# Performance work log

Hardware: AMD Instinct MI355X
Metric: run time of the kernel (lower is better)

## Reference

```python
import jax, jax.numpy as jnp
import numpy as np


def _conv1x1(x, W, b):
    # x: (B,C,H,W), W: (O,C), b: (O,)
    return jnp.einsum('bchw,oc->bohw', x, W) + b[None, :, None, None]


def _maxpool2(x):
    B, C, H, W = x.shape
    return x.reshape(B, C, H // 2, 2, W // 2, 2).max(axis=(3, 5))


def setup_inputs() -> dict:
    key = jax.random.key(0)
    ks = jax.random.split(key, 6)
    B, C, H, W = 8, 1024, 64, 64
    DI, DO = 512, 1024
    std = 0.01  # matches nn.init.normal_(std=0.01)
    return {
        'x': jax.random.normal(ks[0], (B, C, H, W), dtype=jnp.float32),
        'W_theta': std * jax.random.normal(ks[1], (DI, C), dtype=jnp.float32),
        'b_theta': jnp.zeros((DI,), jnp.float32),
        'W_phi': std * jax.random.normal(ks[2], (DI, C), dtype=jnp.float32),
        'b_phi': jnp.zeros((DI,), jnp.float32),
        'W_g': std * jax.random.normal(ks[3], (DI, C), dtype=jnp.float32),
        'b_g': jnp.zeros((DI,), jnp.float32),
        'W_out': std * jax.random.normal(ks[4], (DO, DI), dtype=jnp.float32),
        'b_out': jnp.zeros((DO,), jnp.float32),
    }


def reference(x, W_theta, b_theta, W_phi, b_phi, W_g, b_g, W_out, b_out):
    B, C, H, W = x.shape
    di = W_theta.shape[0]
    scale = di ** (-0.5)
    # queries from full-res map: (B, di, N) with N = H*W
    theta = _conv1x1(x, W_theta, b_theta).reshape(B, di, H * W)
    # keys/values from 2x2-maxpooled map: (B, di, M), M = (H/2)*(W/2)
    px = _maxpool2(x)
    phi = _conv1x1(px, W_phi, b_phi).reshape(B, di, -1)
    g = _conv1x1(px, W_g, b_g).reshape(B, di, -1)
    # attention: (B, N, M)
    logits = jnp.einsum('bdn,bdm->bnm', theta, phi) * scale
    p = jax.nn.softmax(logits, axis=-1)
    # aggregate values: (B, di, N) -> (B, di, H, W)
    t = jnp.einsum('bdm,bnm->bdn', g, p).reshape(B, di, H, W)
    y = _conv1x1(t, W_out, b_out)
    return y + x
```

## Files before the change

### kernel.cpp

```cpp
#include <hip/hip_runtime.h>
#include <hip/hip_bf16.h>
#include <stdint.h>

typedef __bf16 bf16;
typedef __bf16 bf16x8 __attribute__((ext_vector_type(8)));
typedef __bf16 bf16x4 __attribute__((ext_vector_type(4)));
typedef float f32x4 __attribute__((ext_vector_type(4)));

#define GLOAD_LDS16(gptr, lptr)                                                        \
  __builtin_amdgcn_global_load_lds((const __attribute__((address_space(1))) void*)(gptr), \
                                   (__attribute__((address_space(3))) void*)(lptr), 16, 0, 0)

__global__ __launch_bounds__(256) void cast_f2b(const float* __restrict__ in,
                                                bf16* __restrict__ out, int n) {
  int i = (blockIdx.x * 256 + threadIdx.x) * 4;
  if (i >= n) return;
  const float4 v = *(const float4*)(in + i);
  bf16x4 o;
  o[0] = (bf16)v.x; o[1] = (bf16)v.y; o[2] = (bf16)v.z; o[3] = (bf16)v.w;
  *(bf16x4*)(out + i) = o;
}

__global__ __launch_bounds__(256) void prep_kernel(const float* __restrict__ x,
                                                   bf16* __restrict__ xbT,
                                                   bf16* __restrict__ pxT) {
  const int b = blockIdx.y;
  x   += (size_t)b * 1024 * 4096;
  xbT += (size_t)b * 4096 * 1024;
  pxT += (size_t)b * 1024 * 1024;
  const int bid = blockIdx.x;
  const int h0 = bid & 31, ct = bid >> 5;
  const int tid = threadIdx.x;
  __shared__ float tile[32][129];
  const float* xs = x + (size_t)(ct * 32) * 4096 + h0 * 128;
#pragma unroll
  for (int e = 0; e < 16; ++e) {
    int idx = e * 256 + tid;
    int c = idx >> 7, n = idx & 127;
    tile[c][n] = xs[(size_t)c * 4096 + n];
  }
  __syncthreads();
  bf16* xo = xbT + (size_t)(h0 * 128) * 1024 + ct * 32;
#pragma unroll
  for (int e = 0; e < 16; ++e) {
    int idx = e * 256 + tid;
    int n = idx >> 5, c = idx & 31;
    xo[(size_t)n * 1024 + c] = (bf16)tile[c][n];
  }
  bf16* po = pxT + (size_t)(h0 * 32) * 1024 + ct * 32;
#pragma unroll
  for (int e = 0; e < 4; ++e) {
    int idx = e * 256 + tid;
    int m = idx >> 5, c = idx & 31;
    float v = fmaxf(fmaxf(tile[c][2 * m], tile[c][2 * m + 1]),
                    fmaxf(tile[c][64 + 2 * m], tile[c][64 + 2 * m + 1]));
    po[(size_t)m * 1024 + c] = (bf16)v;
  }
}

__global__ __launch_bounds__(256) void rowsum_k(const bf16* __restrict__ P,
                                                float* __restrict__ rs) {
  const int row = blockIdx.x * 4 + (threadIdx.x >> 6);
  const int lane = threadIdx.x & 63;
  const bf16* Pr = P + (size_t)row * 1024;
  bf16x8 v0 = *(const bf16x8*)(Pr + lane * 16);
  bf16x8 v1 = *(const bf16x8*)(Pr + lane * 16 + 8);
  float s = 0.f;
#pragma unroll
  for (int e = 0; e < 8; ++e) s += (float)v0[e] + (float)v1[e];
#pragma unroll
  for (int o = 32; o > 0; o >>= 1) s += __shfl_xor(s, o);
  if (lane == 0) rs[row] = s;
}

template <int EPI>
__global__ __launch_bounds__(512, 1) void gemm256(
    const bf16* __restrict__ A, long long sA, int lda,
    const bf16* __restrict__ B, long long sB, int ldb,
    void* __restrict__ Cv, long long sC, int ldc, int K,
    const float* __restrict__ bias,
    const float* __restrict__ resid, long long sResid, float scale) {
  const int z = blockIdx.z;
  A += (size_t)z * sA;
  B += (size_t)z * sB;
  const int tid = threadIdx.x;
  const int w = tid >> 6, lane = tid & 63;
  const int r16 = lane & 15, q4 = lane >> 4;
  const int wm = w >> 2, wn = w & 3;
  const long long tileM = (long long)blockIdx.x * 256;
  const long long tileN = (long long)blockIdx.y * 256;

  __shared__ bf16 As[4][8192];
  __shared__ bf16 Bs[4][8192];

  f32x4 acc[8][4] = {};

  const int srow = tid >> 2;
  const int skb  = (tid & 3) ^ ((srow >> 1) & 3);
  const char* Ag = (const char*)A + ((size_t)(tileM + srow) * lda + skb * 8) * 2;
  const char* Bg = (const char*)B + ((size_t)(tileN + srow) * ldb + skb * 8) * 2;
  const size_t a128 = (size_t)128 * lda * 2;
  const size_t b128 = (size_t)128 * ldb * 2;

  auto stA = [&](int T) {
    bf16* d = &As[T & 3][w * 512];
    const char* s = Ag + (size_t)T * 64;
    GLOAD_LDS16(s, d);
    GLOAD_LDS16(s + a128, d + 4096);
  };
  auto stB = [&](int T) {
    bf16* d = &Bs[T & 3][w * 512];
    const char* s = Bg + (size_t)T * 64;
    GLOAD_LDS16(s, d);
    GLOAD_LDS16(s + b128, d + 4096);
  };

  stA(0); stB(0); stA(1); stB(1);
  const int NT = K >> 5;

  for (int T = 0; T < NT; ++T) {
    if (T + 2 < NT) stA(T + 2);
    if (T + 2 < NT)      asm volatile("s_waitcnt vmcnt(6)" ::: "memory");
    else if (T + 1 < NT) asm volatile("s_waitcnt vmcnt(4)" ::: "memory");
    else                 asm volatile("s_waitcnt vmcnt(0)" ::: "memory");
    __builtin_amdgcn_s_barrier();
    asm volatile("" ::: "memory");

    const char* Asl = (const char*)&As[T & 3][0];
    const char* Bsl = (const char*)&Bs[T & 3][0];
    bf16x8 bf_[4];
#pragma unroll
    for (int ni = 0; ni < 4; ++ni) {
      const int row = wn * 64 + ni * 16 + r16;
      bf_[ni] = *(const bf16x8*)(Bsl + row * 64 + ((q4 ^ ((row >> 1) & 3)) << 4));
    }
    bf16x8 af[4];
#pragma unroll
    for (int mi = 0; mi < 4; ++mi) {
      const int row = wm * 128 + mi * 16 + r16;
      af[mi] = *(const bf16x8*)(Asl + row * 64 + ((q4 ^ ((row >> 1) & 3)) << 4));
    }
    __builtin_amdgcn_s_setprio(1);
#pragma unroll
    for (int mi = 0; mi < 4; ++mi)
#pragma unroll
      for (int ni = 0; ni < 4; ++ni)
        acc[mi][ni] = __builtin_amdgcn_mfma_f32_16x16x32_bf16(af[mi], bf_[ni], acc[mi][ni], 0, 0, 0);
    __builtin_amdgcn_s_setprio(0);

    if (T + 2 < NT) stB(T + 2);
#pragma unroll
    for (int mi = 0; mi < 4; ++mi) {
      const int row = wm * 128 + 64 + mi * 16 + r16;
      af[mi] = *(const bf16x8*)(Asl + row * 64 + ((q4 ^ ((row >> 1) & 3)) << 4));
    }
    __builtin_amdgcn_s_setprio(1);
#pragma unroll
    for (int mi = 0; mi < 4; ++mi)
#pragma unroll
      for (int ni = 0; ni < 4; ++ni)
        acc[4 + mi][ni] = __builtin_amdgcn_mfma_f32_16x16x32_bf16(af[mi], bf_[ni], acc[4 + mi][ni], 0, 0, 0);
    __builtin_amdgcn_s_setprio(0);
  }

  if constexpr (EPI == 4) {
    float* C = (float*)Cv + (size_t)z * sC;
    const float* rz = resid + (size_t)z * sResid;
#pragma unroll
    for (int a = 0; a < 8; ++a) {
      const int row0 = (int)tileM + wm * 128 + a * 16 + q4 * 4;
#pragma unroll
      for (int ni = 0; ni < 4; ++ni) {
        const int col = (int)tileN + wn * 64 + ni * 16 + r16;
#pragma unroll
        for (int r = 0; r < 4; ++r)
          C[(size_t)(row0 + r) * ldc + col] =
              acc[a][ni][r] + bias[row0 + r] + rz[(size_t)(row0 + r) * ldc + col];
      }
    }
  } else if constexpr (EPI == 5) {
    bf16* C = (bf16*)Cv + (size_t)z * sC;
#pragma unroll
    for (int a = 0; a < 8; ++a) {
      const int row0 = (int)tileM + wm * 128 + a * 16 + q4 * 4;
#pragma unroll
      for (int ni = 0; ni < 4; ++ni) {
        const int col = (int)tileN + wn * 64 + ni * 16 + r16;
#pragma unroll
        for (int r = 0; r < 4; ++r)
          C[(size_t)(row0 + r) * ldc + col] = (bf16)__expf(acc[a][ni][r]);
      }
    }
  } else if constexpr (EPI == 7) {
    bf16* C = (bf16*)Cv + (size_t)z * sC;
    const float* rsp = bias + (size_t)z * 4096;
#pragma unroll
    for (int a = 0; a < 8; ++a) {
      const int row0 = (int)tileM + wm * 128 + a * 16 + q4 * 4;
      float inv[4];
#pragma unroll
      for (int r = 0; r < 4; ++r) inv[r] = 1.0f / rsp[row0 + r];
#pragma unroll
      for (int ni = 0; ni < 4; ++ni) {
        const int col = (int)tileN + wn * 64 + ni * 16 + r16;
#pragma unroll
        for (int r = 0; r < 4; ++r)
          C[(size_t)(row0 + r) * ldc + col] = (bf16)(acc[a][ni][r] * inv[r]);
      }
    }
  } else {
    bf16* C = (bf16*)Cv + (size_t)z * sC;
#pragma unroll
    for (int a = 0; a < 8; ++a) {
      const int row0 = (int)tileM + wm * 128 + a * 16 + q4 * 4;
#pragma unroll
      for (int ni = 0; ni < 4; ++ni) {
        const int col = (int)tileN + wn * 64 + ni * 16 + r16;
        const float badd = bias[col];
#pragma unroll
        for (int r = 0; r < 4; ++r)
          C[(size_t)(row0 + r) * ldc + col] = (bf16)((acc[a][ni][r] + badd) * scale);
      }
    }
  }
}

template <int EPI>
__global__ __launch_bounds__(256) void gemm_bt(
    const bf16* __restrict__ A, long long sA, int lda,
    const bf16* __restrict__ B, long long sB, int ldb,
    void* __restrict__ Cv, long long sC, int ldc, int K,
    const float* __restrict__ bias,
    const float* __restrict__ resid, long long sResid, float scale) {
  const int z = blockIdx.z;
  A += (size_t)z * sA;
  B += (size_t)z * sB;
  const int tid = threadIdx.x;
  const int w = tid >> 6, lane = tid & 63;
  const int r16 = lane & 15, q4 = lane >> 4;
  const long long tileM = (long long)blockIdx.x * 128;
  const long long tileN = (long long)blockIdx.y * 128;

  __shared__ bf16 As[2][128 * 32];
  __shared__ bf16 Bs[2][128 * 32];

  f32x4 acc[4][4] = {};

  const int srow = tid >> 2;
  const int soff = (tid & 3) * 16;
  const char* Ag0 = (const char*)A + ((size_t)(tileM + srow) * lda) * 2 + soff;
  const char* Bg0 = (const char*)B + ((size_t)(tileN + srow) * ldb) * 2 + soff;
  const size_t arow64 = (size_t)64 * lda * 2;
  const size_t brow64 = (size_t)64 * ldb * 2;

  auto stage = [&](int buf, int k0) {
    const char* a = Ag0 + (size_t)k0 * 2;
    const char* b = Bg0 + (size_t)k0 * 2;
    bf16* al = &As[buf][w * 512];
    bf16* bl = &Bs[buf][w * 512];
    GLOAD_LDS16(a, al);
    GLOAD_LDS16(a + arow64, al + 2048);
    GLOAD_LDS16(b, bl);
    GLOAD_LDS16(b + brow64, bl + 2048);
  };

  const int wr = (w >> 1) * 64, wc = (w & 1) * 64;
  const int nt = K >> 5;
  stage(0, 0);
  __syncthreads();
  int cur = 0;
  for (int t = 0; t < nt; ++t) {
    if (t + 1 < nt) stage(cur ^ 1, (t + 1) * 32);
    bf16x8 af[4], bfv[4];
#pragma unroll
    for (int f = 0; f < 4; ++f) {
      af[f]  = *(const bf16x8*)&As[cur][(wr + f * 16 + r16) * 32 + q4 * 8];
      bfv[f] = *(const bf16x8*)&Bs[cur][(wc + f * 16 + r16) * 32 + q4 * 8];
    }
#pragma unroll
    for (int i = 0; i < 4; ++i)
#pragma unroll
      for (int j = 0; j < 4; ++j)
        acc[i][j] = __builtin_amdgcn_mfma_f32_16x16x32_bf16(af[i], bfv[j], acc[i][j], 0, 0, 0);
    __syncthreads();
    cur ^= 1;
  }

  bf16* C = (bf16*)Cv + (size_t)z * sC;
#pragma unroll
  for (int i = 0; i < 4; ++i) {
    const int row0 = (int)tileM + wr + i * 16 + q4 * 4;
#pragma unroll
    for (int j = 0; j < 4; ++j) {
      const int col = (int)tileN + wc + j * 16 + r16;
      float badd = 0.f;
      if constexpr (EPI == 1) badd = bias[col];
#pragma unroll
      for (int r = 0; r < 4; ++r) {
        float v = acc[i][j][r];
        if constexpr (EPI == 1) v = (v + badd) * scale;
        if constexpr (EPI == 2) v += bias[row0 + r];
        C[(size_t)(row0 + r) * ldc + col] = (bf16)v;
      }
    }
  }
}

extern "C" void kernel_launch(void* const* d_in, const int* in_sizes, int n_in,
                              void* d_out, int out_size, void* d_ws, size_t ws_size,
                              hipStream_t stream) {
  const float* x  = (const float*)d_in[0];
  const float* Wt = (const float*)d_in[1];
  const float* bt = (const float*)d_in[2];
  const float* Wp = (const float*)d_in[3];
  const float* bp = (const float*)d_in[4];
  const float* Wg = (const float*)d_in[5];
  const float* bg = (const float*)d_in[6];
  const float* Wo = (const float*)d_in[7];
  const float* bo = (const float*)d_in[8];
  float* out = (float*)d_out;

  const size_t MB = 1024ull * 1024ull;
  char* ws = (char*)d_ws;
  bf16* WtB = (bf16*)(ws + 0 * MB);
  bf16* WpB = (bf16*)(ws + 1 * MB);
  bf16* WgB = (bf16*)(ws + 2 * MB);
  bf16* WoB = (bf16*)(ws + 3 * MB);

  cast_f2b<<<512, 256, 0, stream>>>(Wt, WtB, 512 * 1024);
  cast_f2b<<<512, 256, 0, stream>>>(Wp, WpB, 512 * 1024);
  cast_f2b<<<512, 256, 0, stream>>>(Wg, WgB, 512 * 1024);
  cast_f2b<<<512, 256, 0, stream>>>(Wo, WoB, 1024 * 512);

  const float SCALE = 0.044194173824159216f;

  auto run_g6 = [&](int nb, int b0, bf16* tT) {
    gemm256<4><<<dim3(4, 16, nb), 512, 0, stream>>>(WoB, 0, 512, tT, 4096ll * 512, 512,
                                                    out + (size_t)b0 * 1024 * 4096,
                                                    1024ll * 4096, 4096, 512,
                                                    bo, x + (size_t)b0 * 1024 * 4096,
                                                    1024ll * 4096, 1.f);
  };

  if (ws_size >= 164 * MB) {
    bf16* pxT    = (bf16*)(ws + 4 * MB);
    bf16* phiT   = (bf16*)(ws + 20 * MB);
    bf16* g      = (bf16*)(ws + 28 * MB);
    bf16* thetaT = (bf16*)(ws + 36 * MB);
    bf16* tT     = (bf16*)(ws + 68 * MB);
    bf16* xbT    = (bf16*)(ws + 100 * MB);
    bf16*  Pt   = (bf16*)d_out;
    float* rsum = (float*)((char*)d_out + 80 * MB);

    prep_kernel<<<dim3(1024, 8), 256, 0, stream>>>(x, xbT, pxT);
    gemm256<1><<<dim3(16, 2, 8), 512, 0, stream>>>(xbT, 4096ll * 1024, 1024, WtB, 0, 1024,
                                                   thetaT, 4096ll * 512, 512, 1024,
                                                   bt, nullptr, 0, SCALE);
    gemm_bt<1><<<dim3(8, 4, 8), 256, 0, stream>>>(pxT, 1024ll * 1024, 1024, WpB, 0, 1024,
                                                  phiT, 1024ll * 512, 512, 1024,
                                                  bp, nullptr, 0, 1.f);
    gemm_bt<2><<<dim3(4, 8, 8), 256, 0, stream>>>(WgB, 0, 1024, pxT, 1024ll * 1024, 1024,
                                                  g, 512ll * 1024, 1024, 1024,
                                                  bg, nullptr, 0, 1.f);
    gemm256<5><<<dim3(16, 4, 8), 512, 0, stream>>>(thetaT, 4096ll * 512, 512,
                                                   phiT, 1024ll * 512, 512,
                                                   Pt, 4096ll * 1024, 1024, 512,
                                                   nullptr, nullptr, 0, 1.f);
    rowsum_k<<<8192, 256, 0, stream>>>(Pt, rsum);
    gemm256<7><<<dim3(16, 2, 8), 512, 0, stream>>>(Pt, 4096ll * 1024, 1024,
                                                   g, 512ll * 1024, 1024,
                                                   tT, 4096ll * 512, 512, 1024,
                                                   rsum, nullptr, 0, 1.f);
    run_g6(8, 0, tT);
  } else if (ws_size >= 108 * MB) {
    bf16* pxT    = (bf16*)(ws + 4 * MB);
    bf16* phiT   = (bf16*)(ws + 20 * MB);
    bf16* g      = (bf16*)(ws + 28 * MB);
    bf16* thetaT = (bf16*)(ws + 36 * MB);
    bf16* tT     = (bf16*)(ws + 68 * MB);
    bf16* xbT    = (bf16*)(ws + 100 * MB);
    float* rsum = (float*)((char*)d_out + 80 * MB);
    for (int b = 0; b < 8; ++b) {
      prep_kernel<<<dim3(1024, 1), 256, 0, stream>>>(x + (size_t)b * 1024 * 4096, xbT,
                                                     pxT + (size_t)b * 1024 * 1024);
      gemm256<1><<<dim3(16, 2, 1), 512, 0, stream>>>(xbT, 0, 1024, WtB, 0, 1024,
                                                     thetaT + (size_t)b * 4096 * 512, 0, 512,
                                                     1024, bt, nullptr, 0, SCALE);
    }
    gemm_bt<1><<<dim3(8, 4, 8), 256, 0, stream>>>(pxT, 1024ll * 1024, 1024, WpB, 0, 1024,
                                                  phiT, 1024ll * 512, 512, 1024,
                                                  bp, nullptr, 0, 1.f);
    gemm_bt<2><<<dim3(4, 8, 8), 256, 0, stream>>>(WgB, 0, 1024, pxT, 1024ll * 1024, 1024,
                                                  g, 512ll * 1024, 1024, 1024,
                                                  bg, nullptr, 0, 1.f);
    for (int b = 0; b < 8; ++b) {
      bf16* Ptb = (bf16*)d_out + (size_t)b * 4096 * 1024;
      gemm256<5><<<dim3(16, 4, 1), 512, 0, stream>>>(thetaT + (size_t)b * 4096 * 512, 0, 512,
                                                     phiT + (size_t)b * 1024 * 512, 0, 512,
                                                     Ptb, 0, 1024, 512,
                                                     nullptr, nullptr, 0, 1.f);
      rowsum_k<<<1024, 256, 0, stream>>>(Ptb, rsum + (size_t)b * 4096);
      gemm256<7><<<dim3(16, 2, 1), 512, 0, stream>>>(Ptb, 0, 1024,
                                                     g + (size_t)b * 512 * 1024, 0, 1024,
                                                     tT + (size_t)b * 4096 * 512, 0, 512, 1024,
                                                     rsum + (size_t)b * 4096, nullptr, 0, 1.f);
    }
    run_g6(8, 0, tT);
  } else {
    float* rsum  = (float*)(ws + 4 * MB);
    bf16* pxT    = (bf16*)(ws + 5 * MB);
    bf16* phiT   = (bf16*)(ws + 7 * MB);
    bf16* g      = (bf16*)(ws + 8 * MB);
    bf16* thetaT = (bf16*)(ws + 9 * MB);
    bf16* tT     = (bf16*)(ws + 13 * MB);
    bf16* Pt     = (bf16*)(ws + 17 * MB);
    bf16* xbT    = (bf16*)(ws + 25 * MB);
    for (int b = 0; b < 8; ++b) {
      prep_kernel<<<dim3(1024, 1), 256, 0, stream>>>(x + (size_t)b * 1024 * 4096, xbT, pxT);
      gemm256<1><<<dim3(16, 2, 1), 512, 0, stream>>>(xbT, 0, 1024, WtB, 0, 1024,
                                                     thetaT, 0, 512, 1024,
                                                     bt, nullptr, 0, SCALE);
      gemm_bt<1><<<dim3(8, 4, 1), 256, 0, stream>>>(pxT, 0, 1024, WpB, 0, 1024,
                                                    phiT, 0, 512, 1024,
                                                    bp, nullptr, 0, 1.f);
      gemm_bt<2><<<dim3(4, 8, 1), 256, 0, stream>>>(WgB, 0, 1024, pxT, 0, 1024,
                                                    g, 0, 1024, 1024,
                                                    bg, nullptr, 0, 1.f);
      gemm256<5><<<dim3(16, 4, 1), 512, 0, stream>>>(thetaT, 0, 512, phiT, 0, 512,
                                                     Pt, 0, 1024, 512,
                                                     nullptr, nullptr, 0, 1.f);
      rowsum_k<<<1024, 256, 0, stream>>>(Pt, rsum);
      gemm256<7><<<dim3(16, 2, 1), 512, 0, stream>>>(Pt, 0, 1024, g, 0, 1024,
                                                     tT, 0, 512, 1024,
                                                     rsum, nullptr, 0, 1.f);
      run_g6(1, b, tT);
    }
  }
}
```

Baseline: 322.9 us.

## Shrink gemm256 tile to 128x256, double-buffer, fuse softmax row sums via atomics

The main GEMM kernel moves from 256x256 tiles with a 4-stage LDS ring to 128x256 tiles with a 2-stage buffer, which cuts LDS use and accumulator registers and raises the launch-bounds occupancy hint. Grids are doubled in M to match. The separate rowsum pass over the exp(P) matrix is removed, and row sums are now built in the exp epilogue with shuffle reductions and atomicAdd into a buffer zeroed by a new small kernel. The trade-off is less B-tile reuse per block, a full vmcnt(0) wait each iteration with less prefetch depth, and atomic contention on the row sums.

```diff
diff --git a/kernel.cpp b/kernel.cpp
--- a/kernel.cpp
+++ b/kernel.cpp
@@ -19,6 +19,11 @@
   bf16x4 o;
   o[0] = (bf16)v.x; o[1] = (bf16)v.y; o[2] = (bf16)v.z; o[3] = (bf16)v.w;
   *(bf16x4*)(out + i) = o;
+}
+
+__global__ __launch_bounds__(256) void zero_k(float* __restrict__ p, int n) {
+  int i = blockIdx.x * 256 + threadIdx.x;
+  if (i < n) p[i] = 0.f;
 }
 
 __global__ __launch_bounds__(256) void prep_kernel(const float* __restrict__ x,
@@ -58,28 +63,14 @@
   }
 }
 
-__global__ __launch_bounds__(256) void rowsum_k(const bf16* __restrict__ P,
-                                                float* __restrict__ rs) {
-  const int row = blockIdx.x * 4 + (threadIdx.x >> 6);
-  const int lane = threadIdx.x & 63;
-  const bf16* Pr = P + (size_t)row * 1024;
-  bf16x8 v0 = *(const bf16x8*)(Pr + lane * 16);
-  bf16x8 v1 = *(const bf16x8*)(Pr + lane * 16 + 8);
-  float s = 0.f;
-#pragma unroll
-  for (int e = 0; e < 8; ++e) s += (float)v0[e] + (float)v1[e];
-#pragma unroll
-  for (int o = 32; o > 0; o >>= 1) s += __shfl_xor(s, o);
-  if (lane == 0) rs[row] = s;
-}
-
 template <int EPI>
-__global__ __launch_bounds__(512, 1) void gemm256(
+__global__ __launch_bounds__(512, 4) void gemm256(
     const bf16* __restrict__ A, long long sA, int lda,
     const bf16* __restrict__ B, long long sB, int ldb,
     void* __restrict__ Cv, long long sC, int ldc, int K,
     const float* __restrict__ bias,
-    const float* __restrict__ resid, long long sResid, float scale) {
+    const float* __restrict__ resid, long long sResid, float scale,
+    float* __restrict__ rs_out) {
   const int z = blockIdx.z;
   A += (size_t)z * sA;
   B += (size_t)z * sB;
@@ -87,59 +78,48 @@
   const int w = tid >> 6, lane = tid & 63;
   const int r16 = lane & 15, q4 = lane >> 4;
   const int wm = w >> 2, wn = w & 3;
-  const long long tileM = (long long)blockIdx.x * 256;
+  const long long tileM = (long long)blockIdx.x * 128;
   const long long tileN = (long long)blockIdx.y * 256;
 
-  __shared__ bf16 As[4][8192];
-  __shared__ bf16 Bs[4][8192];
-
-  f32x4 acc[8][4] = {};
+  __shared__ bf16 As[2][4096];
+  __shared__ bf16 Bs[2][8192];
+
+  f32x4 acc[4][4] = {};
 
   const int srow = tid >> 2;
   const int skb  = (tid & 3) ^ ((srow >> 1) & 3);
   const char* Ag = (const char*)A + ((size_t)(tileM + srow) * lda + skb * 8) * 2;
   const char* Bg = (const char*)B + ((size_t)(tileN + srow) * ldb + skb * 8) * 2;
-  const size_t a128 = (size_t)128 * lda * 2;
   const size_t b128 = (size_t)128 * ldb * 2;
 
-  auto stA = [&](int T) {
-    bf16* d = &As[T & 3][w * 512];
-    const char* s = Ag + (size_t)T * 64;
-    GLOAD_LDS16(s, d);
-    GLOAD_LDS16(s + a128, d + 4096);
+  auto stage = [&](int T) {
+    const int sl = T & 1;
+    GLOAD_LDS16(Ag + (size_t)T * 64, &As[sl][w * 512]);
+    GLOAD_LDS16(Bg + (size_t)T * 64, &Bs[sl][w * 512]);
+    GLOAD_LDS16(Bg + (size_t)T * 64 + b128, &Bs[sl][4096 + w * 512]);
   };
-  auto stB = [&](int T) {
-    bf16* d = &Bs[T & 3][w * 512];
-    const char* s = Bg + (size_t)T * 64;
-    GLOAD_LDS16(s, d);
-    GLOAD_LDS16(s + b128, d + 4096);
-  };
-
-  stA(0); stB(0); stA(1); stB(1);
+
+  stage(0);
   const int NT = K >> 5;
 
   for (int T = 0; T < NT; ++T) {
-    if (T + 2 < NT) stA(T + 2);
-    if (T + 2 < NT)      asm volatile("s_waitcnt vmcnt(6)" ::: "memory");
-    else if (T + 1 < NT) asm volatile("s_waitcnt vmcnt(4)" ::: "memory");
-    else                 asm volatile("s_waitcnt vmcnt(0)" ::: "memory");
+    asm volatile("s_waitcnt vmcnt(0)" ::: "memory");
     __builtin_amdgcn_s_barrier();
     asm volatile("" ::: "memory");
-
-    const char* Asl = (const char*)&As[T & 3][0];
-    const char* Bsl = (const char*)&Bs[T & 3][0];
-    bf16x8 bf_[4];
+    if (T + 1 < NT) stage(T + 1);
+    const char* Asl = (const char*)&As[T & 1][0];
+    const char* Bsl = (const char*)&Bs[T & 1][0];
+    bf16x8 af[4], bf_[4];
+#pragma unroll
+    for (int mi = 0; mi < 4; ++mi) {
+      const int row = wm * 64 + mi * 16 + r16;
+      af[mi] = *(const bf16x8*)(Asl + row * 64 + ((q4 ^ ((row >> 1) & 3)) << 4));
+    }
 #pragma unroll
     for (int ni = 0; ni < 4; ++ni) {
       const int row = wn * 64 + ni * 16 + r16;
       bf_[ni] = *(const bf16x8*)(Bsl + row * 64 + ((q4 ^ ((row >> 1) & 3)) << 4));
     }
-    bf16x8 af[4];
-#pragma unroll
-    for (int mi = 0; mi < 4; ++mi) {
-      const int row = wm * 128 + mi * 16 + r16;
-      af[mi] = *(const bf16x8*)(Asl + row * 64 + ((q4 ^ ((row >> 1) & 3)) << 4));
-    }
     __builtin_amdgcn_s_setprio(1);
 #pragma unroll
     for (int mi = 0; mi < 4; ++mi)
@@ -147,28 +127,14 @@
       for (int ni = 0; ni < 4; ++ni)
         acc[mi][ni] = __builtin_amdgcn_mfma_f32_16x16x32_bf16(af[mi], bf_[ni], acc[mi][ni], 0, 0, 0);
     __builtin_amdgcn_s_setprio(0);
-
-    if (T + 2 < NT) stB(T + 2);
-#pragma unroll
-    for (int mi = 0; mi < 4; ++mi) {
-      const int row = wm * 128 + 64 + mi * 16 + r16;
-      af[mi] = *(const bf16x8*)(Asl + row * 64 + ((q4 ^ ((row >> 1) & 3)) << 4));
-    }
-    __builtin_amdgcn_s_setprio(1);
-#pragma unroll
-    for (int mi = 0; mi < 4; ++mi)
-#pragma unroll
-      for (int ni = 0; ni < 4; ++ni)
-        acc[4 + mi][ni] = __builtin_amdgcn_mfma_f32_16x16x32_bf16(af[mi], bf_[ni], acc[4 + mi][ni], 0, 0, 0);
-    __builtin_amdgcn_s_setprio(0);
   }
 
   if constexpr (EPI == 4) {
     float* C = (float*)Cv + (size_t)z * sC;
     const float* rz = resid + (size_t)z * sResid;
 #pragma unroll
-    for (int a = 0; a < 8; ++a) {
-      const int row0 = (int)tileM + wm * 128 + a * 16 + q4 * 4;
+    for (int a = 0; a < 4; ++a) {
+      const int row0 = (int)tileM + wm * 64 + a * 16 + q4 * 4;
 #pragma unroll
       for (int ni = 0; ni < 4; ++ni) {
         const int col = (int)tileN + wn * 64 + ni * 16 + r16;
@@ -180,23 +146,37 @@
     }
   } else if constexpr (EPI == 5) {
     bf16* C = (bf16*)Cv + (size_t)z * sC;
-#pragma unroll
-    for (int a = 0; a < 8; ++a) {
-      const int row0 = (int)tileM + wm * 128 + a * 16 + q4 * 4;
+    float* rsp = rs_out + (size_t)z * 4096;
+#pragma unroll
+    for (int a = 0; a < 4; ++a) {
+      const int row0 = (int)tileM + wm * 64 + a * 16 + q4 * 4;
+      float psum[4] = {0.f, 0.f, 0.f, 0.f};
 #pragma unroll
       for (int ni = 0; ni < 4; ++ni) {
         const int col = (int)tileN + wn * 64 + ni * 16 + r16;
 #pragma unroll
-        for (int r = 0; r < 4; ++r)
-          C[(size_t)(row0 + r) * ldc + col] = (bf16)__expf(acc[a][ni][r]);
+        for (int r = 0; r < 4; ++r) {
+          float e = __expf(acc[a][ni][r]);
+          psum[r] += e;
+          C[(size_t)(row0 + r) * ldc + col] = (bf16)e;
+        }
+      }
+#pragma unroll
+      for (int r = 0; r < 4; ++r) {
+        float v = psum[r];
+        v += __shfl_xor(v, 1);
+        v += __shfl_xor(v, 2);
+        v += __shfl_xor(v, 4);
+        v += __shfl_xor(v, 8);
+        if (r16 == 0) atomicAdd(&rsp[row0 + r], v);
       }
     }
   } else if constexpr (EPI == 7) {
     bf16* C = (bf16*)Cv + (size_t)z * sC;
     const float* rsp = bias + (size_t)z * 4096;
 #pragma unroll
-    for (int a = 0; a < 8; ++a) {
-      const int row0 = (int)tileM + wm * 128 + a * 16 + q4 * 4;
+    for (int a = 0; a < 4; ++a) {
+      const int row0 = (int)tileM + wm * 64 + a * 16 + q4 * 4;
       float inv[4];
 #pragma unroll
       for (int r = 0; r < 4; ++r) inv[r] = 1.0f / rsp[row0 + r];
@@ -211,8 +191,8 @@
   } else {
     bf16* C = (bf16*)Cv + (size_t)z * sC;
 #pragma unroll
-    for (int a = 0; a < 8; ++a) {
-      const int row0 = (int)tileM + wm * 128 + a * 16 + q4 * 4;
+    for (int a = 0; a < 4; ++a) {
+      const int row0 = (int)tileM + wm * 64 + a * 16 + q4 * 4;
 #pragma unroll
       for (int ni = 0; ni < 4; ++ni) {
         const int col = (int)tileN + wn * 64 + ni * 16 + r16;
@@ -230,8 +210,7 @@
     const bf16* __restrict__ A, long long sA, int lda,
     const bf16* __restrict__ B, long long sB, int ldb,
     void* __restrict__ Cv, long long sC, int ldc, int K,
-    const float* __restrict__ bias,
-    const float* __restrict__ resid, long long sResid, float scale) {
+    const float* __restrict__ bias, float scale) {
   const int z = blockIdx.z;
   A += (size_t)z * sA;
   B += (size_t)z * sB;
@@ -335,11 +314,11 @@
   const float SCALE = 0.044194173824159216f;
 
   auto run_g6 = [&](int nb, int b0, bf16* tT) {
-    gemm256<4><<<dim3(4, 16, nb), 512, 0, stream>>>(WoB, 0, 512, tT, 4096ll * 512, 512,
+    gemm256<4><<<dim3(8, 16, nb), 512, 0, stream>>>(WoB, 0, 512, tT, 4096ll * 512, 512,
                                                     out + (size_t)b0 * 1024 * 4096,
                                                     1024ll * 4096, 4096, 512,
                                                     bo, x + (size_t)b0 * 1024 * 4096,
-                                                    1024ll * 4096, 1.f);
+                                                    1024ll * 4096, 1.f, nullptr);
   };
 
   if (ws_size >= 164 * MB) {
@@ -353,24 +332,22 @@
     float* rsum = (float*)((char*)d_out + 80 * MB);
 
     prep_kernel<<<dim3(1024, 8), 256, 0, stream>>>(x, xbT, pxT);
-    gemm256<1><<<dim3(16, 2, 8), 512, 0, stream>>>(xbT, 4096ll * 1024, 1024, WtB, 0, 1024,
+    gemm256<1><<<dim3(32, 2, 8), 512, 0, stream>>>(xbT, 4096ll * 1024, 1024, WtB, 0, 1024,
                                                    thetaT, 4096ll * 512, 512, 1024,
-                                                   bt, nullptr, 0, SCALE);
+                                                   bt, nullptr, 0, SCALE, nullptr);
     gemm_bt<1><<<dim3(8, 4, 8), 256, 0, stream>>>(pxT, 1024ll * 1024, 1024, WpB, 0, 1024,
-                                                  phiT, 1024ll * 512, 512, 1024,
-                                                  bp, nullptr, 0, 1.f);
+                                                  phiT, 1024ll * 512, 512, 1024, bp, 1.f);
     gemm_bt<2><<<dim3(4, 8, 8), 256, 0, stream>>>(WgB, 0, 1024, pxT, 1024ll * 1024, 1024,
-                                                  g, 512ll * 1024, 1024, 1024,
-                                                  bg, nullptr, 0, 1.f);
-    gemm256<5><<<dim3(16, 4, 8), 512, 0, stream>>>(thetaT, 4096ll * 512, 512,
+                                                  g, 512ll * 1024, 1024, 1024, bg, 1.f);
+    zero_k<<<128, 256, 0, stream>>>(rsum, 32768);
+    gemm256<5><<<dim3(32, 4, 8), 512, 0, stream>>>(thetaT, 4096ll * 512, 512,
                                                    phiT, 1024ll * 512, 512,
                                                    Pt, 4096ll * 1024, 1024, 512,
-                                                   nullptr, nullptr, 0, 1.f);
-    rowsum_k<<<8192, 256, 0, stream>>>(Pt, rsum);
-    gemm256<7><<<dim3(16, 2, 8), 512, 0, stream>>>(Pt, 4096ll * 1024, 1024,
+                                                   nullptr, nullptr, 0, 1.f, rsum);
+    gemm256<7><<<dim3(32, 2, 8), 512, 0, stream>>>(Pt, 4096ll * 1024, 1024,
                                                    g, 512ll * 1024, 1024,
                                                    tT, 4096ll * 512, 512, 1024,
-                                                   rsum, nullptr, 0, 1.f);
+                                                   rsum, nullptr, 0, 1.f, nullptr);
     run_g6(8, 0, tT);
   } else if (ws_size >= 108 * MB) {
     bf16* pxT    = (bf16*)(ws + 4 * MB);
@@ -383,27 +360,27 @@
     for (int b = 0; b < 8; ++b) {
       prep_kernel<<<dim3(1024, 1), 256, 0, stream>>>(x + (size_t)b * 1024 * 4096, xbT,
                                                      pxT + (size_t)b * 1024 * 1024);
-      gemm256<1><<<dim3(16, 2, 1), 512, 0, stream>>>(xbT, 0, 1024, WtB, 0, 1024,
+      gemm256<1><<<dim3(32, 2, 1), 512, 0, stream>>>(xbT, 0, 1024, WtB, 0, 1024,
                                                      thetaT + (size_t)b * 4096 * 512, 0, 512,
-                                                     1024, bt, nullptr, 0, SCALE);
+                                                     1024, bt, nullptr, 0, SCALE, nullptr);
     }
     gemm_bt<1><<<dim3(8, 4, 8), 256, 0, stream>>>(pxT, 1024ll * 1024, 1024, WpB, 0, 1024,
-                                                  phiT, 1024ll * 512, 512, 1024,
-                                                  bp, nullptr, 0, 1.f);
+                                                  phiT, 1024ll * 512, 512, 1024, bp, 1.f);
     gemm_bt<2><<<dim3(4, 8, 8), 256, 0, stream>>>(WgB, 0, 1024, pxT, 1024ll * 1024, 1024,
-                                                  g, 512ll * 1024, 1024, 1024,
-                                                  bg, nullptr, 0, 1.f);
+                                                  g, 512ll * 1024, 1024, 1024, bg, 1.f);
     for (int b = 0; b < 8; ++b) {
       bf16* Ptb = (bf16*)d_out + (size_t)b * 4096 * 1024;
-      gemm256<5><<<dim3(16, 4, 1), 512, 0, stream>>>(thetaT + (size_t)b * 4096 * 512, 0, 512,
+      zero_k<<<16, 256, 0, stream>>>(rsum + (size_t)b * 4096, 4096);
+      gemm256<5><<<dim3(32, 4, 1), 512, 0, stream>>>(thetaT + (size_t)b * 4096 * 512, 0, 512,
                                                      phiT + (size_t)b * 1024 * 512, 0, 512,
                                                      Ptb, 0, 1024, 512,
-                                                     nullptr, nullptr, 0, 1.f);
-      rowsum_k<<<1024, 256, 0, stream>>>(Ptb, rsum + (size_t)b * 4096);
-      gemm256<7><<<dim3(16, 2, 1), 512, 0, stream>>>(Ptb, 0, 1024,
+                                                     nullptr, nullptr, 0, 1.f,
+                                                     rsum + (size_t)b * 4096);
+      gemm256<7><<<dim3(32, 2, 1), 512, 0, stream>>>(Ptb, 0, 1024,
                                                      g + (size_t)b * 512 * 1024, 0, 1024,
                                                      tT + (size_t)b * 4096 * 512, 0, 512, 1024,
-                                                     rsum + (size_t)b * 4096, nullptr, 0, 1.f);
+                                                     rsum + (size_t)b * 4096, nullptr, 0, 1.f,
+                                                     nullptr);
     }
     run_g6(8, 0, tT);
   } else {
@@ -417,22 +394,20 @@
     bf16* xbT    = (bf16*)(ws + 25 * MB);
     for (int b = 0; b < 8; ++b) {
       prep_kernel<<<dim3(1024, 1), 256, 0, stream>>>(x + (size_t)b * 1024 * 4096, xbT, pxT);
-      gemm256<1><<<dim3(16, 2, 1), 512, 0, stream>>>(xbT, 0, 1024, WtB, 0, 1024,
+      gemm256<1><<<dim3(32, 2, 1), 512, 0, stream>>>(xbT, 0, 1024, WtB, 0, 1024,
                                                      thetaT, 0, 512, 1024,
-                                                     bt, nullptr, 0, SCALE);
+                                                     bt, nullptr, 0, SCALE, nullptr);
       gemm_bt<1><<<dim3(8, 4, 1), 256, 0, stream>>>(pxT, 0, 1024, WpB, 0, 1024,
-                                                    phiT, 0, 512, 1024,
-                                                    bp, nullptr, 0, 1.f);
+                                                    phiT, 0, 512, 1024, bp, 1.f);
       gemm_bt<2><<<dim3(4, 8, 1), 256, 0, stream>>>(WgB, 0, 1024, pxT, 0, 1024,
-                                                    g, 0, 1024, 1024,
-                                                    bg, nullptr, 0, 1.f);
-      gemm256<5><<<dim3(16, 4, 1), 512, 0, stream>>>(thetaT, 0, 512, phiT, 0, 512,
+                                                    g, 0, 1024, 1024, bg, 1.f);
+      zero_k<<<16, 256, 0, stream>>>(rsum, 4096);
+      gemm256<5><<<dim3(32, 4, 1), 512, 0, stream>>>(thetaT, 0, 512, phiT, 0, 512,
                                                      Pt, 0, 1024, 512,
-                                                     nullptr, nullptr, 0, 1.f);
-      rowsum_k<<<1024, 256, 0, stream>>>(Pt, rsum);
-      gemm256<7><<<dim3(16, 2, 1), 512, 0, stream>>>(Pt, 0, 1024, g, 0, 1024,
+                                                     nullptr, nullptr, 0, 1.f, rsum);
+      gemm256<7><<<dim3(32, 2, 1), 512, 0, stream>>>(Pt, 0, 1024, g, 0, 1024,
                                                      tT, 0, 512, 1024,
-                                                     rsum, nullptr, 0, 1.f);
+                                                     rsum, nullptr, 0, 1.f, nullptr);
       run_g6(1, b, tT);
     }
   }
```

Result: no change. 318.4 us (-1.4%).
